# Kernel optimization log

Hardware: AMD Instinct MI355X
Metric: run time of the kernel (lower is better)

## Reference

```python
import jax, jax.numpy as jnp
import numpy as np

D_MODEL = 1024
N_HEADS = 16
HEAD_DIM = D_MODEL // N_HEADS
WINDOW = 256


def setup_inputs() -> dict:
    key = jax.random.key(0)
    ks = jax.random.split(key, 5)
    s = 1.0 / np.sqrt(D_MODEL)
    x = jax.random.normal(ks[0], (1, 4096, D_MODEL), dtype=jnp.float32)
    W_qkv = jax.random.uniform(ks[1], (D_MODEL, 3 * D_MODEL), jnp.float32, -s, s)
    b_qkv = jax.random.uniform(ks[2], (3 * D_MODEL,), jnp.float32, -s, s)
    W_proj = jax.random.uniform(ks[3], (D_MODEL, D_MODEL), jnp.float32, -s, s)
    b_proj = jax.random.uniform(ks[4], (D_MODEL,), jnp.float32, -s, s)
    return {"x": x, "W_qkv": W_qkv, "b_qkv": b_qkv, "W_proj": W_proj, "b_proj": b_proj}


def reference(x, W_qkv, b_qkv, W_proj, b_proj):
    b, t, c = x.shape
    qkv = x @ W_qkv + b_qkv  # [b,t,3c]
    q, k, v = jnp.split(qkv, 3, axis=-1)
    # [b,h,t,d]
    q = q.reshape(b, t, N_HEADS, HEAD_DIM).transpose(0, 2, 1, 3)
    k = k.reshape(b, t, N_HEADS, HEAD_DIM).transpose(0, 2, 1, 3)
    v = v.reshape(b, t, N_HEADS, HEAD_DIM).transpose(0, 2, 1, 3)
    att = jnp.einsum('bhqd,bhkd->bhqk', q, k) / np.sqrt(HEAD_DIM)
    idx = jnp.arange(t)
    diff = idx[:, None] - idx[None, :]  # query - key
    allowed = (diff >= 0) & (diff < WINDOW)  # causal & local window
    att = jnp.where(allowed[None, None], att, -jnp.inf)
    att = jax.nn.softmax(att, axis=-1)
    y = jnp.einsum('bhqk,bhkd->bhqd', att, v)
    y = y.transpose(0, 2, 1, 3).reshape(b, t, c)
    return y @ W_proj + b_proj
```

## Files before the change

### kernel.cpp

```cpp
#include <hip/hip_runtime.h>
#include <stdint.h>

#define TSEQ 4096
#define DMODEL 1024
#define N3 3072
#define NHEADS 16
#define HDIM 64
#define WINDOW 256

typedef __attribute__((ext_vector_type(8))) short short8;
typedef __attribute__((ext_vector_type(4))) float f32x4;

__device__ __forceinline__ unsigned short f2bf(float f) {
  unsigned u = __builtin_bit_cast(unsigned, f);
  return (unsigned short)((u + 0x7fffu + ((u >> 16) & 1u)) >> 16);
}

__device__ __forceinline__ unsigned cvtpk(float lo, float hi) {
  unsigned r;
  asm("v_cvt_pk_bf16_f32 %0, %1, %2" : "=v"(r) : "v"(lo), "v"(hi));
  return r;
}

__device__ __forceinline__ f32x4 mfma16(short8 a, short8 b, f32x4 c) {
  return __builtin_amdgcn_mfma_f32_16x16x32_bf16(a, b, c, 0, 0, 0);
}

__device__ __forceinline__ void g2lds16(const void* g, void* l) {
  __builtin_amdgcn_global_load_lds(
      (const __attribute__((address_space(1))) void*)(uintptr_t)g,
      (__attribute__((address_space(3))) void*)(uintptr_t)l,
      16, 0, 0);
}


__global__ __launch_bounds__(256) void prep(const float* __restrict__ x,
                                            const float* __restrict__ Wqkv,
                                            const float* __restrict__ Wproj,
                                            unsigned short* __restrict__ xb,
                                            unsigned short* __restrict__ oQkvT,
                                            unsigned short* __restrict__ oProjT) {
  __shared__ float tile[32][33];
  int b = blockIdx.x;
  int tid = threadIdx.x;
  if (b < 4096) {
    int i = (b * 256 + tid) * 4;
    float4 v = *(const float4*)(x + i);
    unsigned lo = cvtpk(v.x, v.y), hi = cvtpk(v.z, v.w);
    unsigned long long packed = (unsigned long long)lo | ((unsigned long long)hi << 32);
    *(unsigned long long*)(xb + i) = packed;
    return;
  }
  b -= 4096;
  int bx = b & 127, by = b >> 7;
  const float* in;
  unsigned short* out;
  int C;
  if (bx < 96) {
    in = Wqkv; out = oQkvT; C = N3;
  } else {
    bx -= 96; in = Wproj; out = oProjT; C = DMODEL;
  }
  const int R = DMODEL;
  int c0 = bx * 32;
  int r0 = by * 32;
  int tx = tid & 31, ty = tid >> 5;
#pragma unroll
  for (int i = 0; i < 32; i += 8)
    tile[ty + i][tx] = in[(size_t)(r0 + ty + i) * C + c0 + tx];
  __syncthreads();
#pragma unroll
  for (int i = 0; i < 32; i += 8)
    out[(size_t)(c0 + ty + i) * R + r0 + tx] = f2bf(tile[tx][ty + i]);
}


template <int EPI, int MI, int NI>
__global__ __launch_bounds__(256)
void gemm_bf16(const unsigned short* __restrict__ A,
               const unsigned short* __restrict__ BT,
               const float* __restrict__ bias,
               unsigned short* __restrict__ oQ,
               unsigned short* __restrict__ oK,
               unsigned short* __restrict__ oVT,
               float* __restrict__ oF) {
  constexpr int BM = MI * 32, BN = NI * 32;
  constexpr int LPS = MI / 2 + NI / 2;
  __shared__ unsigned short Asm[2][BM * 32];
  __shared__ unsigned short Bsm[2][BN * 32];
  const int K = 1024;
  int m0 = blockIdx.x * BM;
  int n0 = blockIdx.y * BN;
  int tid = threadIdx.x;
  int w = tid >> 6, lane = tid & 63;
  int l15 = lane & 15, l4 = lane >> 4;
  int wm = (w >> 1) * (MI * 16), wn = (w & 1) * (NI * 16);

  f32x4 acc[MI][NI];
#pragma unroll
  for (int i = 0; i < MI; i++)
#pragma unroll
    for (int j = 0; j < NI; j++) acc[i][j] = (f32x4){0.f, 0.f, 0.f, 0.f};

  int lr = lane >> 2;
  int slot = ((lane & 3) * 16) ^ (((lr >> 1) & 3) << 4);
  const char* aG = (const char*)(A + (size_t)(m0 + w * (MI * 8) + lr) * K) + slot;
  const char* bG = (const char*)(BT + (size_t)(n0 + w * (NI * 8) + lr) * K) + slot;

  auto stage = [&](int s, int b) {
    int koff = s * 64;
#pragma unroll
    for (int c = 0; c < MI / 2; c++)
      g2lds16(aG + (size_t)c * 16 * 2048 + koff, &Asm[b][(w * (MI / 2) + c) * 512]);
#pragma unroll
    for (int j = 0; j < NI / 2; j++)
      g2lds16(bG + (size_t)j * 16 * 2048 + koff, &Bsm[b][(w * (NI / 2) + j) * 512]);
  };

  int sX = ((l15 >> 1) & 3) << 4;

  auto compute = [&](int b) {
    short8 af[MI], bfr[NI];
#pragma unroll
    for (int mi = 0; mi < MI; mi++) {
      int rA = wm + mi * 16 + l15;
      af[mi] = *(const short8*)((const char*)Asm[b] + rA * 64 + ((l4 * 16) ^ sX));
    }
#pragma unroll
    for (int ni = 0; ni < NI; ni++) {
      int rB = wn + ni * 16 + l15;
      bfr[ni] = *(const short8*)((const char*)Bsm[b] + rB * 64 + ((l4 * 16) ^ sX));
    }
#pragma unroll
    for (int mi = 0; mi < MI; mi++)
#pragma unroll
      for (int ni = 0; ni < NI; ni++)
        acc[mi][ni] = mfma16(af[mi], bfr[ni], acc[mi][ni]);
  };

  const int NS = K / 32;
  stage(0, 0);
#pragma unroll 1
  for (int s = 0; s < NS; s++) {
    if (s + 1 < NS) {
      stage(s + 1, (s + 1) & 1);
      if constexpr (LPS == 4) asm volatile("s_waitcnt vmcnt(4)" ::: "memory");
      else asm volatile("s_waitcnt vmcnt(2)" ::: "memory");
    } else {
      asm volatile("s_waitcnt vmcnt(0)" ::: "memory");
    }
    __builtin_amdgcn_s_barrier();
    __builtin_amdgcn_sched_barrier(0);
    compute(s & 1);
    __builtin_amdgcn_sched_barrier(0);
    __builtin_amdgcn_s_barrier();
  }

#pragma unroll
  for (int ni = 0; ni < NI; ni++) {
    int nn = n0 + wn + ni * 16 + l15;
    float bv = bias[nn];
    int c = nn & 1023;
    int hh = c >> 6, dd = c & 63;
#pragma unroll
    for (int mi = 0; mi < MI; mi++) {
      int mm = m0 + wm + mi * 16 + l4 * 4;
      float v0 = acc[mi][ni][0] + bv;
      float v1 = acc[mi][ni][1] + bv;
      float v2 = acc[mi][ni][2] + bv;
      float v3 = acc[mi][ni][3] + bv;
      if (EPI == 1) {
        oF[(size_t)(mm + 0) * 1024 + nn] = v0;
        oF[(size_t)(mm + 1) * 1024 + nn] = v1;
        oF[(size_t)(mm + 2) * 1024 + nn] = v2;
        oF[(size_t)(mm + 3) * 1024 + nn] = v3;
      } else if (nn < 1024) {
        oQ[((size_t)hh * TSEQ + mm + 0) * 64 + dd] = f2bf(v0 * 0.125f);
        oQ[((size_t)hh * TSEQ + mm + 1) * 64 + dd] = f2bf(v1 * 0.125f);
        oQ[((size_t)hh * TSEQ + mm + 2) * 64 + dd] = f2bf(v2 * 0.125f);
        oQ[((size_t)hh * TSEQ + mm + 3) * 64 + dd] = f2bf(v3 * 0.125f);
      } else if (nn < 2048) {
        oK[((size_t)hh * TSEQ + mm + 0) * 64 + dd] = f2bf(v0);
        oK[((size_t)hh * TSEQ + mm + 1) * 64 + dd] = f2bf(v1);
        oK[((size_t)hh * TSEQ + mm + 2) * 64 + dd] = f2bf(v2);
        oK[((size_t)hh * TSEQ + mm + 3) * 64 + dd] = f2bf(v3);
      } else {
        unsigned lo = cvtpk(v0, v1), hi = cvtpk(v2, v3);
        unsigned long long pv = (unsigned long long)lo | ((unsigned long long)hi << 32);
        *(unsigned long long*)(oVT + ((size_t)hh * 64 + dd) * TSEQ + mm) = pv;
      }
    }
  }
}


__global__ __launch_bounds__(512)
void attn_swa(const unsigned short* __restrict__ Qa,
              const unsigned short* __restrict__ Ka,
              const unsigned short* __restrict__ Vt,
              unsigned short* __restrict__ Y) {
  __shared__ __align__(16) char KV[2][16384];
  __shared__ __align__(16) unsigned char Pl[8][2048];
  int flat = blockIdx.x;
  int swz = (flat & 7) * 64 + (flat >> 3);
  int h = swz >> 5, qb2 = swz & 31;
  int w = threadIdx.x >> 6, lane = threadIdx.x & 63;
  int l15 = lane & 15, l4 = lane >> 4;
  int g = w >> 2, wv = w & 3;
  int qb = qb2 * 2 + g;
  int qrow0 = qb * 64 + wv * 16;
  int q = qrow0 + l15;

  const unsigned short* qp = Qa + ((size_t)h * TSEQ + q) * 64 + l4 * 8;
  short8 qf0 = *(const short8*)qp;
  short8 qf1 = *(const short8*)(qp + 32);

  const char* kgb = (const char*)(Ka + (size_t)h * TSEQ * 64);
  const char* vgb = (const char*)(Vt + (size_t)h * 64 * TSEQ);

  int sub8 = lane >> 3, slot = (lane & 7) * 16;
  int r8 = w * 8 + sub8;
  auto stage = [&](int kt, int b) {
    int kbase = kt * 64;
    g2lds16(kgb + (size_t)(kbase + r8) * 128 + (slot ^ (sub8 << 4)), &KV[b][w * 1024]);
    g2lds16(vgb + (size_t)r8 * 8192 + (size_t)kbase * 2 + (slot ^ (sub8 << 4)),
            &KV[b][8192 + w * 1024]);
  };

  float m = -1e30f, lsum = 0.f;
  f32x4 o[4];
#pragma unroll
  for (int ni = 0; ni < 4; ni++) o[ni] = (f32x4){0.f, 0.f, 0.f, 0.f};

  unsigned char* pw = Pl[w];
  int xw = (l15 & 7) << 4;

  auto compute = [&](int kt, int b, int MODE) {
    int kbase = kt * 64;
    const char* kb = KV[b];
    const char* vb = KV[b] + 8192;
    f32x4 s[4];
    __builtin_amdgcn_s_setprio(1);
#pragma unroll
    for (int ni = 0; ni < 4; ni++) {
      int rb = (ni * 16 + l15) * 128;
      short8 k0 = *(const short8*)(kb + rb + ((l4 * 16) ^ xw));
      short8 k1 = *(const short8*)(kb + rb + ((64 + l4 * 16) ^ xw));
      f32x4 z = (f32x4){0.f, 0.f, 0.f, 0.f};
      z = mfma16(k0, qf0, z);
      s[ni] = mfma16(k1, qf1, z);
    }
    __builtin_amdgcn_s_setprio(0);
    if (MODE != 0) {
#pragma unroll
      for (int ni = 0; ni < 4; ni++)
#pragma unroll
        for (int r = 0; r < 4; r++) {
          int key = kbase + ni * 16 + l4 * 4 + r;
          bool ok = (MODE == 2) ? (key <= q) : (q - key < WINDOW);
          s[ni][r] = ok ? s[ni][r] : -1e30f;
        }
    }
    float pm0 = fmaxf(fmaxf(s[0][0], s[0][1]), fmaxf(s[0][2], s[0][3]));
    float pm1 = fmaxf(fmaxf(s[1][0], s[1][1]), fmaxf(s[1][2], s[1][3]));
    float pm2 = fmaxf(fmaxf(s[2][0], s[2][1]), fmaxf(s[2][2], s[2][3]));
    float pm3 = fmaxf(fmaxf(s[3][0], s[3][1]), fmaxf(s[3][2], s[3][3]));
    float pm = fmaxf(fmaxf(pm0, pm1), fmaxf(pm2, pm3));
    pm = fmaxf(pm, __shfl_xor(pm, 16, 64));
    pm = fmaxf(pm, __shfl_xor(pm, 32, 64));
    if (!__all(pm <= m)) {
      float mn = fmaxf(m, pm);
      float alpha = __expf(m - mn);
      m = mn;
      lsum *= alpha;
#pragma unroll
      for (int ni = 0; ni < 4; ni++)
#pragma unroll
        for (int r = 0; r < 4; r++) o[ni][r] *= alpha;
    }
    float rs = 0.f;
#pragma unroll
    for (int ni = 0; ni < 4; ni++)
#pragma unroll
      for (int r = 0; r < 4; r++) {
        float p = __expf(s[ni][r] - m);
        s[ni][r] = p;
        rs += p;
      }
    rs += __shfl_xor(rs, 16, 64);
    rs += __shfl_xor(rs, 32, 64);
    lsum += rs;
#pragma unroll
    for (int ni = 0; ni < 4; ni++) {
      unsigned lo = cvtpk(s[ni][0], s[ni][1]);
      unsigned hi = cvtpk(s[ni][2], s[ni][3]);
      unsigned long long pv = (unsigned long long)lo | ((unsigned long long)hi << 32);
      *(unsigned long long*)(pw + l15 * 128 + ((ni * 32 + l4 * 8) ^ xw)) = pv;
    }
    short8 pa0 = *(const short8*)(pw + l15 * 128 + ((l4 * 16) ^ xw));
    short8 pa1 = *(const short8*)(pw + l15 * 128 + ((64 + l4 * 16) ^ xw));
    __builtin_amdgcn_s_setprio(1);
#pragma unroll
    for (int ni = 0; ni < 4; ni++) {
      int rb = (ni * 16 + l15) * 128;
      short8 v0 = *(const short8*)(vb + rb + ((l4 * 16) ^ xw));
      short8 v1 = *(const short8*)(vb + rb + ((64 + l4 * 16) ^ xw));
      o[ni] = mfma16(v0, pa0, o[ni]);
      o[ni] = mfma16(v1, pa1, o[ni]);
    }
    __builtin_amdgcn_s_setprio(0);
  };

  int qbA = qb2 * 2, qbB = qbA + 1;
  int ktLo = qbA >= 4 ? qbA - 4 : 0;
  int NT = qbB - ktLo + 1;
  stage(ktLo, 0);
  for (int t = 0; t < NT; t++) {
    int kt = ktLo + t;
    if (t + 1 < NT) {
      stage(kt + 1, (t + 1) & 1);
      asm volatile("s_waitcnt vmcnt(2)" ::: "memory");
    } else {
      asm volatile("s_waitcnt vmcnt(0)" ::: "memory");
    }
    __builtin_amdgcn_s_barrier();
    __builtin_amdgcn_sched_barrier(0);
    bool active = (g == 0) ? (kt <= qbA) : (kt >= qbB - 4);
    if (active) {
      int MODE = (kt == qb) ? 2 : ((qb >= 4 && kt == qb - 4) ? 1 : 0);
      compute(kt, t & 1, MODE);
    }
    __builtin_amdgcn_sched_barrier(0);
    __builtin_amdgcn_s_barrier();
  }

  float inv = 1.f / lsum;
#pragma unroll
  for (int ni = 0; ni < 4; ni++) {
    unsigned lo = cvtpk(o[ni][0] * inv, o[ni][1] * inv);
    unsigned hi = cvtpk(o[ni][2] * inv, o[ni][3] * inv);
    unsigned long long yv = (unsigned long long)lo | ((unsigned long long)hi << 32);
    *(unsigned long long*)(Y + (size_t)q * DMODEL + h * 64 + ni * 16 + l4 * 4) = yv;
  }
}


extern "C" void kernel_launch(void* const* d_in, const int* in_sizes, int n_in,
                              void* d_out, int out_size, void* d_ws, size_t ws_size,
                              hipStream_t stream) {
  const float* x = (const float*)d_in[0];
  const float* Wqkv = (const float*)d_in[1];
  const float* bqkv = (const float*)d_in[2];
  const float* Wproj = (const float*)d_in[3];
  const float* bproj = (const float*)d_in[4];
  float* out = (float*)d_out;

  unsigned short* ws = (unsigned short*)d_ws;
  unsigned short* xb = ws;
  unsigned short* wqkvT = xb + (size_t)TSEQ * DMODEL;
  unsigned short* wprojT = wqkvT + (size_t)N3 * DMODEL;
  unsigned short* qarr = wprojT + (size_t)DMODEL * DMODEL;
  unsigned short* karr = qarr + (size_t)NHEADS * TSEQ * HDIM;
  unsigned short* vtarr = karr + (size_t)NHEADS * TSEQ * HDIM;
  unsigned short* yarr = vtarr + (size_t)NHEADS * TSEQ * HDIM;

  prep<<<8192, 256, 0, stream>>>(x, Wqkv, Wproj, xb, wqkvT, wprojT);
  gemm_bf16<0, 4, 4><<<dim3(TSEQ / 128, N3 / 128), 256, 0, stream>>>(
      xb, wqkvT, bqkv, qarr, karr, vtarr, nullptr);
  attn_swa<<<512, 512, 0, stream>>>(qarr, karr, vtarr, yarr);
  gemm_bf16<1, 2, 2><<<dim3(TSEQ / 64, DMODEL / 64), 256, 0, stream>>>(
      yarr, wprojT, bproj, nullptr, nullptr, nullptr, out);
}
```

Baseline: 83.82 us.

## Add dedicated 256x256-tile QKV GEMM kernel with 512 threads and swizzled LDS

```diff
diff --git a/kernel.cpp b/kernel.cpp
--- a/kernel.cpp
+++ b/kernel.cpp
@@ -72,6 +72,124 @@
 #pragma unroll
   for (int i = 0; i < 32; i += 8)
     out[(size_t)(c0 + ty + i) * R + r0 + tx] = f2bf(tile[tx][ty + i]);
+}
+
+
+__global__ __launch_bounds__(512, 2)
+void gemm_qkv_256(const unsigned short* __restrict__ A,
+                  const unsigned short* __restrict__ BT,
+                  const float* __restrict__ bias,
+                  unsigned short* __restrict__ oQ,
+                  unsigned short* __restrict__ oK,
+                  unsigned short* __restrict__ oVT) {
+  __shared__ unsigned short Asm[2][256 * 64];
+  __shared__ unsigned short Bsm[2][256 * 64];
+  int m0 = blockIdx.x * 256;
+  int n0 = blockIdx.y * 256;
+  int tid = threadIdx.x;
+  int w = tid >> 6, lane = tid & 63;
+  int l15 = lane & 15, l4 = lane >> 4;
+  int wr = w >> 2, wc = w & 3;
+
+  f32x4 acc[8][4];
+#pragma unroll
+  for (int i = 0; i < 8; i++)
+#pragma unroll
+    for (int j = 0; j < 4; j++) acc[i][j] = (f32x4){0.f, 0.f, 0.f, 0.f};
+
+  int r8 = lane >> 3;
+  int sslot = ((lane & 7) ^ r8) * 16;
+  const char* aBase = (const char*)A + (size_t)(m0 + r8) * 2048 + sslot;
+  const char* bBase = (const char*)BT + (size_t)(n0 + r8) * 2048 + sslot;
+
+  auto stage = [&](int T, int b) {
+    int koff = T * 128;
+#pragma unroll
+    for (int u = 0; u < 2; u++)
+#pragma unroll
+      for (int j = 0; j < 2; j++) {
+        int R0 = u * 128 + w * 16 + j * 8;
+        g2lds16(aBase + (size_t)R0 * 2048 + koff, &Asm[b][R0 * 64]);
+        g2lds16(bBase + (size_t)R0 * 2048 + koff, &Bsm[b][R0 * 64]);
+      }
+  };
+
+  int xw = (l15 & 7) << 4;
+
+  auto computeIter = [&](int b) {
+    const char* Ab = (const char*)Asm[b];
+    const char* Bb = (const char*)Bsm[b];
+    short8 bfr[4][2];
+#pragma unroll
+    for (int ni = 0; ni < 4; ni++) {
+      int rb = (wc * 64 + ni * 16 + l15) * 128;
+#pragma unroll
+      for (int ks = 0; ks < 2; ks++)
+        bfr[ni][ks] = *(const short8*)(Bb + rb + ((ks * 64 + l4 * 16) ^ xw));
+    }
+#pragma unroll
+    for (int p = 0; p < 4; p++) {
+      short8 af[2][2];
+#pragma unroll
+      for (int i = 0; i < 2; i++) {
+        int ra = (wr * 128 + (p * 2 + i) * 16 + l15) * 128;
+#pragma unroll
+        for (int ks = 0; ks < 2; ks++)
+          af[i][ks] = *(const short8*)(Ab + ra + ((ks * 64 + l4 * 16) ^ xw));
+      }
+      __builtin_amdgcn_s_setprio(1);
+#pragma unroll
+      for (int i = 0; i < 2; i++)
+#pragma unroll
+        for (int ni = 0; ni < 4; ni++) {
+          acc[p * 2 + i][ni] = mfma16(af[i][0], bfr[ni][0], acc[p * 2 + i][ni]);
+          acc[p * 2 + i][ni] = mfma16(af[i][1], bfr[ni][1], acc[p * 2 + i][ni]);
+        }
+      __builtin_amdgcn_s_setprio(0);
+      __builtin_amdgcn_sched_barrier(0);
+    }
+  };
+
+  const int NT = 16;
+  stage(0, 0);
+#pragma unroll 1
+  for (int T = 0; T < NT; T++) {
+    asm volatile("s_waitcnt vmcnt(0)" ::: "memory");
+    __builtin_amdgcn_s_barrier();
+    if (T + 1 < NT) stage(T + 1, (T + 1) & 1);
+    computeIter(T & 1);
+  }
+
+#pragma unroll
+  for (int ni = 0; ni < 4; ni++) {
+    int nn = n0 + wc * 64 + ni * 16 + l15;
+    float bv = bias[nn];
+    int c = nn & 1023;
+    int hh = c >> 6, dd = c & 63;
+#pragma unroll
+    for (int mi = 0; mi < 8; mi++) {
+      int mm = m0 + wr * 128 + mi * 16 + l4 * 4;
+      float v0 = acc[mi][ni][0] + bv;
+      float v1 = acc[mi][ni][1] + bv;
+      float v2 = acc[mi][ni][2] + bv;
+      float v3 = acc[mi][ni][3] + bv;
+      if (nn < 1024) {
+        oQ[((size_t)hh * TSEQ + mm + 0) * 64 + dd] = f2bf(v0 * 0.125f);
+        oQ[((size_t)hh * TSEQ + mm + 1) * 64 + dd] = f2bf(v1 * 0.125f);
+        oQ[((size_t)hh * TSEQ + mm + 2) * 64 + dd] = f2bf(v2 * 0.125f);
+        oQ[((size_t)hh * TSEQ + mm + 3) * 64 + dd] = f2bf(v3 * 0.125f);
+      } else if (nn < 2048) {
+        oK[((size_t)hh * TSEQ + mm + 0) * 64 + dd] = f2bf(v0);
+        oK[((size_t)hh * TSEQ + mm + 1) * 64 + dd] = f2bf(v1);
+        oK[((size_t)hh * TSEQ + mm + 2) * 64 + dd] = f2bf(v2);
+        oK[((size_t)hh * TSEQ + mm + 3) * 64 + dd] = f2bf(v3);
+      } else {
+        unsigned lo = cvtpk(v0, v1), hi = cvtpk(v2, v3);
+        unsigned long long pv = (unsigned long long)lo | ((unsigned long long)hi << 32);
+        *(unsigned long long*)(oVT + ((size_t)hh * 64 + dd) * TSEQ + mm) = pv;
+      }
+    }
+  }
 }
 
 
@@ -160,35 +278,12 @@
   for (int ni = 0; ni < NI; ni++) {
     int nn = n0 + wn + ni * 16 + l15;
     float bv = bias[nn];
-    int c = nn & 1023;
-    int hh = c >> 6, dd = c & 63;
 #pragma unroll
     for (int mi = 0; mi < MI; mi++) {
       int mm = m0 + wm + mi * 16 + l4 * 4;
-      float v0 = acc[mi][ni][0] + bv;
-      float v1 = acc[mi][ni][1] + bv;
-      float v2 = acc[mi][ni][2] + bv;
-      float v3 = acc[mi][ni][3] + bv;
-      if (EPI == 1) {
-        oF[(size_t)(mm + 0) * 1024 + nn] = v0;
-        oF[(size_t)(mm + 1) * 1024 + nn] = v1;
-        oF[(size_t)(mm + 2) * 1024 + nn] = v2;
-        oF[(size_t)(mm + 3) * 1024 + nn] = v3;
-      } else if (nn < 1024) {
-        oQ[((size_t)hh * TSEQ + mm + 0) * 64 + dd] = f2bf(v0 * 0.125f);
-        oQ[((size_t)hh * TSEQ + mm + 1) * 64 + dd] = f2bf(v1 * 0.125f);
-        oQ[((size_t)hh * TSEQ + mm + 2) * 64 + dd] = f2bf(v2 * 0.125f);
-        oQ[((size_t)hh * TSEQ + mm + 3) * 64 + dd] = f2bf(v3 * 0.125f);
-      } else if (nn < 2048) {
-        oK[((size_t)hh * TSEQ + mm + 0) * 64 + dd] = f2bf(v0);
-        oK[((size_t)hh * TSEQ + mm + 1) * 64 + dd] = f2bf(v1);
-        oK[((size_t)hh * TSEQ + mm + 2) * 64 + dd] = f2bf(v2);
-        oK[((size_t)hh * TSEQ + mm + 3) * 64 + dd] = f2bf(v3);
-      } else {
-        unsigned lo = cvtpk(v0, v1), hi = cvtpk(v2, v3);
-        unsigned long long pv = (unsigned long long)lo | ((unsigned long long)hi << 32);
-        *(unsigned long long*)(oVT + ((size_t)hh * 64 + dd) * TSEQ + mm) = pv;
-      }
+#pragma unroll
+      for (int r = 0; r < 4; r++)
+        oF[(size_t)(mm + r) * 1024 + nn] = acc[mi][ni][r] + bv;
     }
   }
 }
@@ -365,8 +460,8 @@
   unsigned short* yarr = vtarr + (size_t)NHEADS * TSEQ * HDIM;
 
   prep<<<8192, 256, 0, stream>>>(x, Wqkv, Wproj, xb, wqkvT, wprojT);
-  gemm_bf16<0, 4, 4><<<dim3(TSEQ / 128, N3 / 128), 256, 0, stream>>>(
-      xb, wqkvT, bqkv, qarr, karr, vtarr, nullptr);
+  gemm_qkv_256<<<dim3(TSEQ / 256, N3 / 256), 512, 0, stream>>>(
+      xb, wqkvT, bqkv, qarr, karr, vtarr);
   attn_swa<<<512, 512, 0, stream>>>(qarr, karr, vtarr, yarr);
   gemm_bf16<1, 2, 2><<<dim3(TSEQ / 64, DMODEL / 64), 256, 0, stream>>>(
       yarr, wprojT, bproj, nullptr, nullptr, nullptr, out);
```

Result: no change. 84.65 us (+1.0%).
